# Kernel tuning notes

Measured on AMD Instinct MI355X. Metric: run time of the kernel, lower is better.

Reference implementation:

```python
import jax, jax.numpy as jnp
import numpy as np


def setup_inputs() -> dict:
    key = jax.random.key(0)
    ks = jax.random.split(key, 7)
    n, d_in, d_h = 1024, 1024, 512
    scale = 1.0 / np.sqrt(d_in)
    return {
        "vectors": jax.random.normal(ks[0], (n, d_in), dtype=jnp.float32),
        "W_h": jax.random.normal(ks[1], (d_h, d_in), dtype=jnp.float32) * scale,
        "b_h": jax.random.normal(ks[2], (d_h,), dtype=jnp.float32) * 0.01,
        "W_m": jax.random.normal(ks[3], (d_h, d_in), dtype=jnp.float32) * scale,
        "b_m": jax.random.normal(ks[4], (d_h,), dtype=jnp.float32) * 0.01,
        "w2": jax.random.normal(ks[5], (d_h,), dtype=jnp.float32) * (1.0 / np.sqrt(d_h)),
        "b2": jax.random.normal(ks[6], (1,), dtype=jnp.float32) * 0.01,
    }


def reference(vectors, W_h, b_h, W_m, b_m, w2, b2):
    # Two linear projections: [n, d_h]
    h = vectors @ W_h.T + b_h  # head representations
    m = vectors @ W_m.T + b_m  # modifier representations
    # Pairwise broadcast add: pair[i, j, :] = h[i] + m[j]  -> [n, n, d_h]
    pair = jnp.tanh(h[:, None, :] + m[None, :, :])
    # Linear to scalar + squeeze -> [n, n]
    scores = jnp.einsum("ijh,h->ij", pair, w2) + b2[0]
    return scores
```

## Files before the change

kernel.cpp:

```cpp
#include <hip/hip_runtime.h>
#include <hip/hip_bf16.h>

#define D_IN  1024
#define D_H   512
#define L2E2  2.885390081777927f
#define ECLAMP 15.0f

typedef _Float16 half8 __attribute__((ext_vector_type(8)));
typedef _Float16 half4v __attribute__((ext_vector_type(4)));
typedef float f32x4 __attribute__((ext_vector_type(4)));

__global__ __launch_bounds__(256) void cvt_kernel(
    const float* __restrict__ V,
    const float* __restrict__ Wh, const float* __restrict__ Wm,
    _Float16* __restrict__ Vh, _Float16* __restrict__ Wf)
{
  const int idx = blockIdx.x * 256 + threadIdx.x;
  {
    float4 x = ((const float4*)V)[idx];
    half4v o = { (_Float16)x.x, (_Float16)x.y, (_Float16)x.z, (_Float16)x.w };
    ((half4v*)Vh)[idx] = o;
  }
  {
    const float4* p = (idx < 131072) ? ((const float4*)Wh + idx)
                                     : ((const float4*)Wm + (idx - 131072));
    float4 x = *p;
    half4v o = { (_Float16)x.x, (_Float16)x.y, (_Float16)x.z, (_Float16)x.w };
    ((half4v*)Wf)[idx] = o;
  }
}

__global__ __launch_bounds__(256, 4) void proj_mfma_kernel(
    const _Float16* __restrict__ Vh, const _Float16* __restrict__ Wf,
    const float* __restrict__ bh, const float* __restrict__ bm,
    float* __restrict__ C)
{
  __shared__ float red[4][32][34];

  const int tid  = threadIdx.x;
  const int lane = tid & 63;
  const int wid  = tid >> 6;
  const int bid  = blockIdx.x;
  const int swz  = (bid & 7) * 128 + (bid >> 3);
  const int i0   = (swz & 31) * 32;
  const int j0   = (swz >> 5) * 32;
  const int r16  = lane & 15;
  const int kg   = lane >> 4;
  const int kb   = wid * 256;

  const _Float16* A0 = Vh + (size_t)(i0 + r16) * 1024 + kb + kg*8;
  const _Float16* A1 = A0 + 16 * 1024;
  const _Float16* B0 = Wf + (size_t)(j0 + r16) * 1024 + kb + kg*8;
  const _Float16* B1 = B0 + 16 * 1024;

  f32x4 acc00 = {0.f,0.f,0.f,0.f}, acc01 = acc00, acc10 = acc00, acc11 = acc00;
  #pragma unroll 4
  for (int k0 = 0; k0 < 256; k0 += 32) {
    half8 a0 = *(const half8*)(A0 + k0);
    half8 a1 = *(const half8*)(A1 + k0);
    half8 b0 = *(const half8*)(B0 + k0);
    half8 b1 = *(const half8*)(B1 + k0);
    acc00 = __builtin_amdgcn_mfma_f32_16x16x32_f16(a0, b0, acc00, 0, 0, 0);
    acc01 = __builtin_amdgcn_mfma_f32_16x16x32_f16(a0, b1, acc01, 0, 0, 0);
    acc10 = __builtin_amdgcn_mfma_f32_16x16x32_f16(a1, b0, acc10, 0, 0, 0);
    acc11 = __builtin_amdgcn_mfma_f32_16x16x32_f16(a1, b1, acc11, 0, 0, 0);
  }

  #pragma unroll
  for (int fi = 0; fi < 2; ++fi) {
    #pragma unroll
    for (int fj = 0; fj < 2; ++fj) {
      const f32x4 acc = (fi == 0) ? (fj == 0 ? acc00 : acc01)
                                  : (fj == 0 ? acc10 : acc11);
      #pragma unroll
      for (int rr = 0; rr < 4; ++rr)
        red[wid][16*fi + 4*kg + rr][16*fj + r16] = acc[rr];
    }
  }
  __syncthreads();

  const int row = tid >> 3;
  const int c4  = (tid & 7) * 4;
  const float* biasp = (j0 < D_H) ? (bh + j0) : (bm + (j0 - D_H));
  float4 bias = *(const float4*)(biasp + c4);
  float4 o;
  #pragma unroll
  for (int q = 0; q < 4; ++q) {
    float s = red[0][row][c4+q] + red[1][row][c4+q]
            + red[2][row][c4+q] + red[3][row][c4+q];
    float x = (s + (&bias.x)[q]) * L2E2;
    x = fminf(fmaxf(x, -ECLAMP), ECLAMP);
    (&o.x)[q] = __builtin_amdgcn_exp2f(x);
  }
  *(float4*)(C + (size_t)(i0 + row) * 1024 + j0 + c4) = o;
}

__global__ __launch_bounds__(256) void proj_kernel(
    const float* __restrict__ V,
    const float* __restrict__ Wh, const float* __restrict__ bh,
    const float* __restrict__ Wm, const float* __restrict__ bm,
    float* __restrict__ C)
{
  __shared__ float As[16][68];
  __shared__ float Bs[16][68];

  const int tid = threadIdx.x;
  const int i0  = (blockIdx.x & 15) * 64, j0 = (blockIdx.x >> 4) * 64;
  const int ti  = tid >> 4, tj = tid & 15;
  const int sr  = tid >> 2;
  const int sk  = (tid & 3) << 2;

  const float* Wbase = (j0 < D_H) ? (Wh + (size_t)j0 * D_IN)
                                  : (Wm + (size_t)(j0 - D_H) * D_IN);
  const float* biasp = (j0 < D_H) ? (bh + j0) : (bm + (j0 - D_H));

  const float* arow = V     + (size_t)(i0 + sr) * D_IN + sk;
  const float* brow = Wbase + (size_t)sr        * D_IN + sk;

  float acc[4][4] = {};
  for (int k0 = 0; k0 < D_IN; k0 += 16) {
    float4 av = *(const float4*)(arow + k0);
    float4 bv = *(const float4*)(brow + k0);
    As[sk+0][sr] = av.x; As[sk+1][sr] = av.y; As[sk+2][sr] = av.z; As[sk+3][sr] = av.w;
    Bs[sk+0][sr] = bv.x; Bs[sk+1][sr] = bv.y; Bs[sk+2][sr] = bv.z; Bs[sk+3][sr] = bv.w;
    __syncthreads();
    #pragma unroll
    for (int kk = 0; kk < 16; ++kk) {
      float4 a = *(const float4*)&As[kk][4*ti];
      float4 b = *(const float4*)&Bs[kk][4*tj];
      #pragma unroll
      for (int x = 0; x < 4; ++x)
        #pragma unroll
        for (int y = 0; y < 4; ++y)
          acc[x][y] = fmaf((&a.x)[x], (&b.x)[y], acc[x][y]);
    }
    __syncthreads();
  }

  const int jl = 4 * tj;
  #pragma unroll
  for (int aa = 0; aa < 4; ++aa) {
    const int i = i0 + 4*ti + aa;
    float4 o;
    #pragma unroll
    for (int bb = 0; bb < 4; ++bb) {
      float x = (acc[aa][bb] + biasp[jl+bb]) * L2E2;
      x = fminf(fmaxf(x, -ECLAMP), ECLAMP);
      (&o.x)[bb] = __builtin_amdgcn_exp2f(x);
    }
    *(float4*)(C + (size_t)i * 1024 + j0 + jl) = o;
  }
}

__global__ __launch_bounds__(256) void score_q_kernel(
    const float* __restrict__ C,
    const float* __restrict__ w2,
    const float* __restrict__ b2,
    _Float16* __restrict__ P0, _Float16* __restrict__ P1,
    _Float16* __restrict__ P2, _Float16* __restrict__ P3)
{
  __shared__ float hs[2][64][36];
  __shared__ float ms[2][64][36];
  __shared__ float wred[4];

  const int tid  = threadIdx.x;
  const int b    = blockIdx.x;
  const int v    = (b & 7) * 128 + (b >> 3);
  const int tile = v >> 2;
  const int kh   = v & 3;
  const int i0   = (tile & 15) * 64;
  const int j0   = (tile >> 4) * 64;
  const int kb   = kh * 128;
  const int ti   = tid >> 4, tj = tid & 15;

  const int sr   = tid >> 3;
  const int sk   = (tid & 7) << 2;

  if (kh == 0) {
    float sw = 0.f;
    for (int t = tid; t < D_H; t += 256) sw += w2[t];
    #pragma unroll
    for (int off = 32; off > 0; off >>= 1) sw += __shfl_down(sw, off, 64);
    if ((tid & 63) == 0) wred[tid >> 6] = sw;
  }

  const float* hrow0 = C + (size_t)(i0 + sr)      * 1024 + kb + sk;
  const float* hrow1 = C + (size_t)(i0 + sr + 32) * 1024 + kb + sk;
  const float* mrow0 = C + (size_t)(j0 + sr)      * 1024 + D_H + kb + sk;
  const float* mrow1 = C + (size_t)(j0 + sr + 32) * 1024 + D_H + kb + sk;

  float4 hv0 = *(const float4*)(hrow0);
  float4 hv1 = *(const float4*)(hrow1);
  float4 mv0 = *(const float4*)(mrow0);
  float4 mv1 = *(const float4*)(mrow1);

  float acc[4][4] = {};
  int p = 0;

  float4 ehA[4], emA[4], ehB[4], emB[4];

  #define LOADG(EH, EM, KK)                                            \
  {                                                                    \
    _Pragma("unroll")                                                  \
    for (int a = 0; a < 4; ++a)                                        \
      (EH)[a] = *(const float4*)&hs[p][ti + 16*a][(KK)];               \
    _Pragma("unroll")                                                  \
    for (int c = 0; c < 4; ++c)                                        \
      (EM)[c] = *(const float4*)&ms[p][tj + 16*c][(KK)];               \
  }

  #define COMPG(EH, EM, KB)                                            \
  {                                                                    \
    const float wA = w2[(KB) + 0];                                     \
    const float wB = w2[(KB) + 1];                                     \
    const float wC = w2[(KB) + 2];                                     \
    const float wD = w2[(KB) + 3];                                     \
    _Pragma("unroll")                                                  \
    for (int a = 0; a < 4; ++a) {                                      \
      _Pragma("unroll")                                                \
      for (int c = 0; c < 4; ++c) {                                    \
        float uA = fmaf((EH)[a].x, (EM)[c].x, 1.f);                    \
        float uB = fmaf((EH)[a].y, (EM)[c].y, 1.f);                    \
        float uC = fmaf((EH)[a].z, (EM)[c].z, 1.f);                    \
        float uD = fmaf((EH)[a].w, (EM)[c].w, 1.f);                    \
        float dAB = uA * uB, dCD = uC * uD;                            \
        float nAB = fmaf(wB, uA, wA * uB);                             \
        float nCD = fmaf(wD, uC, wC * uD);                             \
        float den = dAB * dCD;                                         \
        float num = fmaf(nCD, dAB, nAB * dCD);                         \
        acc[a][c] = fmaf(num, __builtin_amdgcn_rcpf(den), acc[a][c]);  \
      }                                                                \
    }                                                                  \
  }

  for (int k0 = 0; k0 < 128; k0 += 32) {
    *(float4*)&hs[p][sr][sk]      = hv0;
    *(float4*)&hs[p][sr + 32][sk] = hv1;
    *(float4*)&ms[p][sr][sk]      = mv0;
    *(float4*)&ms[p][sr + 32][sk] = mv1;
    __syncthreads();

    if (k0 + 32 < 128) {
      hv0 = *(const float4*)(hrow0 + k0 + 32);
      hv1 = *(const float4*)(hrow1 + k0 + 32);
      mv0 = *(const float4*)(mrow0 + k0 + 32);
      mv1 = *(const float4*)(mrow1 + k0 + 32);
    }

    LOADG(ehA, emA, 0)
    #pragma unroll
    for (int gp = 0; gp < 4; ++gp) {
      const int kk = 8 * gp;
      LOADG(ehB, emB, kk + 4)
      COMPG(ehA, emA, kb + k0 + kk)
      if (gp < 3) { LOADG(ehA, emA, kk + 8) }
      COMPG(ehB, emB, kb + k0 + kk + 4)
    }
    p ^= 1;
  }
  #undef LOADG
  #undef COMPG

  float base = 0.f;
  if (kh == 0) base = b2[0] + wred[0] + wred[1] + wred[2] + wred[3];
  _Float16* Pz = (kh == 0) ? P0 : (kh == 1) ? P1 : (kh == 2) ? P2 : P3;
  #pragma unroll
  for (int a = 0; a < 4; ++a) {
    const int i = i0 + ti + 16*a;
    #pragma unroll
    for (int c = 0; c < 4; ++c) {
      const int j = j0 + tj + 16*c;
      Pz[(size_t)i * 1024 + j] = (_Float16)fmaf(-2.f, acc[a][c], base);
    }
  }
}

__global__ __launch_bounds__(256) void combine_kernel(
    const _Float16* __restrict__ P0, const _Float16* __restrict__ P1,
    const _Float16* __restrict__ P2, const _Float16* __restrict__ P3,
    float* __restrict__ out)
{
  const int idx = blockIdx.x * 256 + threadIdx.x;
  half4v a = ((const half4v*)P0)[idx];
  half4v b = ((const half4v*)P1)[idx];
  half4v c = ((const half4v*)P2)[idx];
  half4v d = ((const half4v*)P3)[idx];
  float4 o;
  #pragma unroll
  for (int q = 0; q < 4; ++q)
    (&o.x)[q] = (float)a[q] + (float)b[q] + ((float)c[q] + (float)d[q]);
  ((float4*)out)[idx] = o;
}

__global__ __launch_bounds__(256, 2) void score_kernel_r9(
    const float* __restrict__ C,
    const float* __restrict__ w2,
    const float* __restrict__ b2,
    float* __restrict__ out)
{
  __shared__ float hs[2][64][36];
  __shared__ float ms[2][32][36];
  __shared__ float wred[4];

  const int tid = threadIdx.x;
  const int bi  = blockIdx.x & 15;
  const int bj  = blockIdx.x >> 4;
  const int i0  = bi * 64, j0 = bj * 32;
  const int ti  = tid >> 4, tj = tid & 15;

  const int sr  = tid >> 3;
  const int sk  = (tid & 7) << 2;

  float sw = 0.f;
  for (int t = tid; t < D_H; t += 256) sw += w2[t];
  #pragma unroll
  for (int off = 32; off > 0; off >>= 1) sw += __shfl_down(sw, off, 64);
  if ((tid & 63) == 0) wred[tid >> 6] = sw;

  const float* hrow0 = C + (size_t)(i0 + sr)      * 1024 + sk;
  const float* hrow1 = C + (size_t)(i0 + sr + 32) * 1024 + sk;
  const float* mrow  = C + (size_t)(j0 + sr) * 1024 + D_H + sk;

  float4 hv0 = *(const float4*)(hrow0);
  float4 hv1 = *(const float4*)(hrow1);
  float4 mv  = *(const float4*)(mrow);

  float acc[4][2] = {};
  int p = 0;

  float4 ehA[4], emA[2], ehB[4], emB[2];

  #define LOADG(EH, EM, KK)                                            \
  {                                                                    \
    _Pragma("unroll")                                                  \
    for (int a = 0; a < 4; ++a)                                        \
      (EH)[a] = *(const float4*)&hs[p][ti + 16*a][(KK)];               \
    _Pragma("unroll")                                                  \
    for (int c = 0; c < 2; ++c)                                        \
      (EM)[c] = *(const float4*)&ms[p][tj + 16*c][(KK)];               \
  }

  #define COMPG(EH, EM, KB)                                            \
  {                                                                    \
    const float wA = w2[(KB) + 0];                                     \
    const float wB = w2[(KB) + 1];                                     \
    const float wC = w2[(KB) + 2];                                     \
    const float wD = w2[(KB) + 3];                                     \
    _Pragma("unroll")                                                  \
    for (int a = 0; a < 4; ++a) {                                      \
      _Pragma("unroll")                                                \
      for (int c = 0; c < 2; ++c) {                                    \
        float uA = fmaf((EH)[a].x, (EM)[c].x, 1.f);                    \
        float uB = fmaf((EH)[a].y, (EM)[c].y, 1.f);                    \
        float uC = fmaf((EH)[a].z, (EM)[c].z, 1.f);                    \
        float uD = fmaf((EH)[a].w, (EM)[c].w, 1.f);                    \
        float dAB = uA * uB, dCD = uC * uD;                            \
        float nAB = fmaf(wB, uA, wA * uB);                             \
        float nCD = fmaf(wD, uC, wC * uD);                             \
        float den = dAB * dCD;                                         \
        float num = fmaf(nCD, dAB, nAB * dCD);                         \
        acc[a][c] = fmaf(num, __builtin_amdgcn_rcpf(den), acc[a][c]);  \
      }                                                                \
    }                                                                  \
  }

  for (int k0 = 0; k0 < D_H; k0 += 32) {
    *(float4*)&hs[p][sr][sk]      = hv0;
    *(float4*)&hs[p][sr + 32][sk] = hv1;
    *(float4*)&ms[p][sr][sk]      = mv;
    __syncthreads();

    if (k0 + 32 < D_H) {
      hv0 = *(const float4*)(hrow0 + k0 + 32);
      hv1 = *(const float4*)(hrow1 + k0 + 32);
      mv  = *(const float4*)(mrow  + k0 + 32);
    }

    LOADG(ehA, emA, 0)
    #pragma unroll
    for (int gp = 0; gp < 4; ++gp) {
      const int kk = 8 * gp;
      LOADG(ehB, emB, kk + 4)
      COMPG(ehA, emA, k0 + kk)
      if (gp < 3) { LOADG(ehA, emA, kk + 8) }
      COMPG(ehB, emB, k0 + kk + 4)
    }
    p ^= 1;
  }
  #undef LOADG
  #undef COMPG

  const float base = b2[0] + wred[0] + wred[1] + wred[2] + wred[3];
  #pragma unroll
  for (int a = 0; a < 4; ++a) {
    const int i = i0 + ti + 16*a;
    #pragma unroll
    for (int c = 0; c < 2; ++c) {
      const int j = j0 + tj + 16*c;
      out[(size_t)i * 1024 + j] = fmaf(-2.f, acc[a][c], base);
    }
  }
}

extern "C" void kernel_launch(void* const* d_in, const int* in_sizes, int n_in,
                              void* d_out, int out_size, void* d_ws, size_t ws_size,
                              hipStream_t stream) {
  const float* V  = (const float*)d_in[0];
  const float* Wh = (const float*)d_in[1];
  const float* bh = (const float*)d_in[2];
  const float* Wm = (const float*)d_in[3];
  const float* bm = (const float*)d_in[4];
  const float* w2 = (const float*)d_in[5];
  const float* b2 = (const float*)d_in[6];
  float* outp = (float*)d_out;

  char* ws = (char*)d_ws;
  float* C = (float*)ws;

  if (ws_size >= (size_t)(16u << 20)) {
    _Float16* Vh = (_Float16*)(ws + (4u << 20));
    _Float16* Wf = (_Float16*)(ws + (6u << 20));
    _Float16* P0 = (_Float16*)(ws + (8u << 20));
    _Float16* P1 = (_Float16*)(ws + (10u << 20));
    _Float16* P2 = (_Float16*)(ws + (12u << 20));
    _Float16* P3 = (_Float16*)(ws + (14u << 20));
    cvt_kernel<<<dim3(1024), dim3(256), 0, stream>>>(V, Wh, Wm, Vh, Wf);
    proj_mfma_kernel<<<dim3(1024), dim3(256), 0, stream>>>(Vh, Wf, bh, bm, C);
    score_q_kernel<<<dim3(1024), dim3(256), 0, stream>>>(C, w2, b2, P0, P1, P2, P3);
    combine_kernel<<<dim3(1024), dim3(256), 0, stream>>>(P0, P1, P2, P3, outp);
  } else if (ws_size >= (size_t)(8u << 20)) {
    _Float16* Vh = (_Float16*)(ws + (4u << 20));
    _Float16* Wf = (_Float16*)(ws + (6u << 20));
    cvt_kernel<<<dim3(1024), dim3(256), 0, stream>>>(V, Wh, Wm, Vh, Wf);
    proj_mfma_kernel<<<dim3(1024), dim3(256), 0, stream>>>(Vh, Wf, bh, bm, C);
    score_kernel_r9<<<dim3(512), dim3(256), 0, stream>>>(C, w2, b2, outp);
  } else {
    proj_kernel<<<dim3(256), dim3(256), 0, stream>>>(V, Wh, bh, Wm, bm, C);
    score_kernel_r9<<<dim3(512), dim3(256), 0, stream>>>(C, w2, b2, outp);
  }
}
```

Measured before the change: 77.12 us.

## Load full 128-wide K slice into shared memory once instead of double-buffered chunks

Replaces the 4-step double-buffered pipeline over 32-wide K chunks with one up-front load of the whole 64x128 h and m tiles into shared memory, followed by a single barrier and a 16-step compute loop. This removes the per-chunk barriers and register staging of the next chunk. In exchange, shared memory per block grows to about 67 KB, which may reduce occupancy, and the global-load latency is no longer overlapped with compute.

```diff
diff --git a/kernel.cpp b/kernel.cpp
--- a/kernel.cpp
+++ b/kernel.cpp
@@ -159,8 +159,8 @@
     _Float16* __restrict__ P0, _Float16* __restrict__ P1,
     _Float16* __restrict__ P2, _Float16* __restrict__ P3)
 {
-  __shared__ float hs[2][64][36];
-  __shared__ float ms[2][64][36];
+  __shared__ float hs[64][132];
+  __shared__ float ms[64][132];
   __shared__ float wred[4];
 
   const int tid  = threadIdx.x;
@@ -173,9 +173,6 @@
   const int kb   = kh * 128;
   const int ti   = tid >> 4, tj = tid & 15;
 
-  const int sr   = tid >> 3;
-  const int sk   = (tid & 7) << 2;
-
   if (kh == 0) {
     float sw = 0.f;
     for (int t = tid; t < D_H; t += 256) sw += w2[t];
@@ -184,29 +181,29 @@
     if ((tid & 63) == 0) wred[tid >> 6] = sw;
   }
 
-  const float* hrow0 = C + (size_t)(i0 + sr)      * 1024 + kb + sk;
-  const float* hrow1 = C + (size_t)(i0 + sr + 32) * 1024 + kb + sk;
-  const float* mrow0 = C + (size_t)(j0 + sr)      * 1024 + D_H + kb + sk;
-  const float* mrow1 = C + (size_t)(j0 + sr + 32) * 1024 + D_H + kb + sk;
-
-  float4 hv0 = *(const float4*)(hrow0);
-  float4 hv1 = *(const float4*)(hrow1);
-  float4 mv0 = *(const float4*)(mrow0);
-  float4 mv1 = *(const float4*)(mrow1);
+  #pragma unroll
+  for (int s = 0; s < 8; ++s) {
+    const int idx = tid + 256 * s;
+    const int row = idx >> 5;
+    const int c4  = (idx & 31) << 2;
+    float4 hv = *(const float4*)(C + (size_t)(i0 + row) * 1024 + kb + c4);
+    float4 mv = *(const float4*)(C + (size_t)(j0 + row) * 1024 + D_H + kb + c4);
+    *(float4*)&hs[row][c4] = hv;
+    *(float4*)&ms[row][c4] = mv;
+  }
+  __syncthreads();
 
   float acc[4][4] = {};
-  int p = 0;
-
   float4 ehA[4], emA[4], ehB[4], emB[4];
 
   #define LOADG(EH, EM, KK)                                            \
   {                                                                    \
     _Pragma("unroll")                                                  \
     for (int a = 0; a < 4; ++a)                                        \
-      (EH)[a] = *(const float4*)&hs[p][ti + 16*a][(KK)];               \
+      (EH)[a] = *(const float4*)&hs[ti + 16*a][(KK)];                  \
     _Pragma("unroll")                                                  \
     for (int c = 0; c < 4; ++c)                                        \
-      (EM)[c] = *(const float4*)&ms[p][tj + 16*c][(KK)];               \
+      (EM)[c] = *(const float4*)&ms[tj + 16*c][(KK)];                  \
   }
 
   #define COMPG(EH, EM, KB)                                            \
@@ -233,30 +230,14 @@
     }                                                                  \
   }
 
-  for (int k0 = 0; k0 < 128; k0 += 32) {
-    *(float4*)&hs[p][sr][sk]      = hv0;
-    *(float4*)&hs[p][sr + 32][sk] = hv1;
-    *(float4*)&ms[p][sr][sk]      = mv0;
-    *(float4*)&ms[p][sr + 32][sk] = mv1;
-    __syncthreads();
-
-    if (k0 + 32 < 128) {
-      hv0 = *(const float4*)(hrow0 + k0 + 32);
-      hv1 = *(const float4*)(hrow1 + k0 + 32);
-      mv0 = *(const float4*)(mrow0 + k0 + 32);
-      mv1 = *(const float4*)(mrow1 + k0 + 32);
-    }
-
-    LOADG(ehA, emA, 0)
-    #pragma unroll
-    for (int gp = 0; gp < 4; ++gp) {
-      const int kk = 8 * gp;
-      LOADG(ehB, emB, kk + 4)
-      COMPG(ehA, emA, kb + k0 + kk)
-      if (gp < 3) { LOADG(ehA, emA, kk + 8) }
-      COMPG(ehB, emB, kb + k0 + kk + 4)
-    }
-    p ^= 1;
+  LOADG(ehA, emA, 0)
+  #pragma unroll 4
+  for (int gp = 0; gp < 16; ++gp) {
+    const int kk = 8 * gp;
+    LOADG(ehB, emB, kk + 4)
+    COMPG(ehA, emA, kb + kk)
+    if (gp < 15) { LOADG(ehA, emA, kk + 8) }
+    COMPG(ehB, emB, kb + kk + 4)
   }
   #undef LOADG
   #undef COMPG
```

Result: slower. 85.75 us (+11.2%).
